# Kernel optimization log

Hardware: AMD Instinct MI355X
Metric: run time of the kernel (lower is better)

The kernel has to match this reference:

```python
import jax, jax.numpy as jnp
import numpy as np


def _glorot(key, shape):
    fan_in, fan_out = shape[0], shape[1]
    lim = float(np.sqrt(6.0 / (fan_in + fan_out)))
    return jax.random.uniform(key, shape, jnp.float32, -lim, lim)


def setup_inputs() -> dict:
    key = jax.random.key(0)
    ks = jax.random.split(key, 17)
    B, P, F = 32, 9045, 750  # batch, pairs-per-subject, feature dim
    x = jax.random.normal(ks[0], (B, P, F), jnp.float32)
    # SimilarityMeasureNetwork: 750 -> 32 -> 16 -> 8 -> 1
    sw1 = _glorot(ks[1], (750, 32)); sb1 = jnp.zeros((32,), jnp.float32)
    sw2 = _glorot(ks[2], (32, 16));  sb2 = jnp.zeros((16,), jnp.float32)
    sw3 = _glorot(ks[3], (16, 8));   sb3 = jnp.zeros((8,), jnp.float32)
    sw4 = _glorot(ks[4], (8, 1));    sb4 = jnp.zeros((1,), jnp.float32)
    # ClassificationNet: 9045 -> 1024 -> 256 -> 64 -> 3
    cw1 = _glorot(ks[5], (9045, 1024)); cb1 = jnp.zeros((1024,), jnp.float32)
    cw2 = _glorot(ks[6], (1024, 256));  cb2 = jnp.zeros((256,), jnp.float32)
    cw3 = _glorot(ks[7], (256, 64));    cb3 = jnp.zeros((64,), jnp.float32)
    cw4 = _glorot(ks[8], (64, 3));      cb4 = jnp.zeros((3,), jnp.float32)
    return dict(x=x, sw1=sw1, sb1=sb1, sw2=sw2, sb2=sb2, sw3=sw3, sb3=sb3,
                sw4=sw4, sb4=sb4, cw1=cw1, cb1=cb1, cw2=cw2, cb2=cb2,
                cw3=cw3, cb3=cb3, cw4=cw4, cb4=cb4)


def reference(x, sw1, sb1, sw2, sb2, sw3, sb3, sw4, sb4,
              cw1, cb1, cw2, cb2, cw3, cb3, cw4, cb4):
    # Similarity MLP, batched over all (subject, pair) rows at once.
    # Dropout layers are identity at inference.
    h = jax.nn.relu(jnp.einsum('bpf,fk->bpk', x, sw1) + sb1)   # [B,P,32]
    h = jax.nn.relu(h @ sw2 + sb2)                              # [B,P,16]
    h = jax.nn.relu(h @ sw3 + sb3)                              # [B,P,8]
    sim = jnp.tanh(h @ sw4 + sb4)[..., 0]                        # [B,P]
    # Classification MLP on the per-subject similarity vector.
    c = jax.nn.relu(sim @ cw1 + cb1)                             # [B,1024]
    c = jax.nn.relu(c @ cw2 + cb2)                               # [B,256]
    c = jax.nn.relu(c @ cw3 + cb3)                               # [B,64]
    logits = c @ cw4 + cb4                                       # [B,3]
    return jax.nn.log_softmax(logits, axis=1)
```

## Files before the change

kernel.cpp:

```cpp
#include <hip/hip_runtime.h>
#include <stdint.h>
#include <stddef.h>

#define BB 32
#define PP 9045
#define FF 750
#define MM (BB*PP)
#define NT16 (MM/16)

typedef float  f32x4  __attribute__((ext_vector_type(4)));
typedef short  s16x8  __attribute__((ext_vector_type(8)));
typedef unsigned int u32x4v __attribute__((ext_vector_type(4)));

typedef const __attribute__((address_space(1))) void* gp1;
typedef __attribute__((address_space(3))) void* sp3;
typedef __attribute__((address_space(3))) unsigned char* sp3c;

__device__ __forceinline__ unsigned rne_bf16(float f){
    unsigned u = __builtin_bit_cast(unsigned, f);
    return (u + 0x7fffu + ((u >> 16) & 1u)) >> 16;
}
__device__ __forceinline__ unsigned pack2(float lo, float hi){
    return rne_bf16(lo) | (rne_bf16(hi) << 16);
}
__device__ __forceinline__ unsigned cvtpk(float lo, float hi){
    unsigned r;
    asm volatile("v_cvt_pk_bf16_f32 %0, %1, %2" : "=v"(r) : "v"(lo), "v"(hi));
    return r;
}
__device__ __forceinline__ float tanh_fast(float v){
    return 1.f - 2.f / (1.f + __expf(2.f * v));
}

__global__ void k_w1f(const float* __restrict__ sw1, u32x4v* __restrict__ w1f){
    int t = blockIdx.x * blockDim.x + threadIdx.x;
    if (t >= 24*2*64) return;
    int lane = t & 63, nt = (t >> 6) & 1, s = t >> 7;
    int col = nt*16 + (lane & 15);
    int kb  = s*32 + ((lane >> 4) << 3);
    float v[8];
    #pragma unroll
    for (int e = 0; e < 8; ++e){ int k = kb + e; v[e] = (k < FF) ? sw1[k*32 + col] : 0.f; }
    u32x4v o;
    o.x = pack2(v[0],v[1]); o.y = pack2(v[2],v[3]);
    o.z = pack2(v[4],v[5]); o.w = pack2(v[6],v[7]);
    w1f[t] = o;
}

__global__ __launch_bounds__(256) void k_sim(
    const float* __restrict__ x, const u32x4v* __restrict__ w1f,
    const float* __restrict__ sb1,
    const float* __restrict__ sw2, const float* __restrict__ sb2,
    const float* __restrict__ sw3, const float* __restrict__ sb3,
    const float* __restrict__ sw4, const float* __restrict__ sb4,
    float* __restrict__ simT)
{
    __shared__ __attribute__((aligned(16))) unsigned char scratch[4*6144];
    const int wid  = threadIdx.x >> 6;
    const int lane = threadIdx.x & 63;
    const int tile = blockIdx.x*4 + wid;
    if (tile >= NT16) return;
    const int g = lane >> 4;
    const int c = lane & 15;
    const int r0 = tile << 4;
    const unsigned wbase = (unsigned)wid * 6144u;

    u32x4v t2, t3;
    {
        float v[8];
        #pragma unroll
        for (int e = 0; e < 8; ++e) v[e] = sw2[(8*g+e)*16 + c];
        t2.x = pack2(v[0],v[1]); t2.y = pack2(v[2],v[3]);
        t2.z = pack2(v[4],v[5]); t2.w = pack2(v[6],v[7]);
        #pragma unroll
        for (int e = 0; e < 8; ++e){
            int k = 8*g+e;
            v[e] = (k < 16 && c < 8) ? sw3[k*8 + c] : 0.f;
        }
        t3.x = pack2(v[0],v[1]); t3.y = pack2(v[2],v[3]);
        t3.z = pack2(v[4],v[5]); t3.w = pack2(v[6],v[7]);
    }
    const s16x8 w2f = __builtin_bit_cast(s16x8, t2);
    const s16x8 w3f = __builtin_bit_cast(s16x8, t3);
    const float w4c  = (c < 8) ? sw4[c] : 0.f;
    const float sb4v = sb4[0];
    const float b2c  = sb2[c];
    const float b3c  = (c < 8) ? sb3[c] : 0.f;

    f32x4 acc0, acc1;
    { float b0 = sb1[c], b1 = sb1[16+c];
      acc0 = (f32x4){b0,b0,b0,b0}; acc1 = (f32x4){b1,b1,b1,b1}; }

    const int rr = lane >> 3;
    const unsigned so = (unsigned)(((lane & 7) << 4) ^ ((rr & 3) << 4));
    const char* src0 = (const char*)x + (size_t)(r0 + rr) * 3000u + so;
    const char* src1 = src0 + 24000;

    unsigned char* ldsg = scratch;
    const uint32_t lbase = (uint32_t)(uintptr_t)(sp3c)scratch;
    const uint32_t sw = ((uint32_t)(c & 3)) << 4;
    const uint32_t rb0 = lbase + wbase + (uint32_t)c*128u + ((32u*(uint32_t)g) ^ sw);
    const uint32_t rb1 = lbase + wbase + (uint32_t)c*128u + (((32u*(uint32_t)g) + 16u) ^ sw);

    const unsigned long long wbw = (unsigned long long)(uintptr_t)w1f + (unsigned)lane*16u;

    u32x4v WA[3], WB[3];

#define GLLP(BUFOFS, STEP) do{ \
    __builtin_amdgcn_global_load_lds((gp1)(src0 + 128*(STEP)), (sp3)(ldsg + wbase + (BUFOFS)), 16, 0, 0); \
    __builtin_amdgcn_global_load_lds((gp1)(src1 + 128*(STEP)), (sp3)(ldsg + wbase + (BUFOFS) + 1024), 16, 0, 0); \
}while(0)

#define W1FLD(SLOT, STEP) do{ \
    unsigned long long wa_ = wbw + (unsigned)(2048*(STEP)); \
    asm volatile("global_load_dwordx4 %0, %1, off" : "=&v"(WA[SLOT]) : "v"(wa_)); \
    asm volatile("global_load_dwordx4 %0, %1, off offset:1024" : "=&v"(WB[SLOT]) : "v"(wa_)); \
}while(0)

#define PACK_MFMA(D0, D1, SLOT) do{ \
    u32x4v a_; \
    a_.x = cvtpk((D0)[0], (D0)[1]); a_.y = cvtpk((D0)[2], (D0)[3]); \
    a_.z = cvtpk((D1)[0], (D1)[1]); a_.w = cvtpk((D1)[2], (D1)[3]); \
    s16x8 av_ = __builtin_bit_cast(s16x8, a_); \
    acc0 = __builtin_amdgcn_mfma_f32_16x16x32_bf16(av_, __builtin_bit_cast(s16x8, WA[SLOT]), acc0, 0,0,0); \
    acc1 = __builtin_amdgcn_mfma_f32_16x16x32_bf16(av_, __builtin_bit_cast(s16x8, WB[SLOT]), acc1, 0,0,0); \
}while(0)

    GLLP(0,    0);
    W1FLD(0,   0);
    GLLP(2048, 1);
    W1FLD(1,   1);
    GLLP(4096, 2);

#pragma unroll
    for (int s = 0; s < 21; ++s){
        asm volatile("s_waitcnt vmcnt(6)");
        f32x4 d0, d1;
        const uint32_t off = (uint32_t)((s % 3) * 2048);
        asm volatile("ds_read_b128 %0, %1" : "=v"(d0) : "v"(rb0 + off));
        asm volatile("ds_read_b128 %0, %1" : "=v"(d1) : "v"(rb1 + off));
        W1FLD((s + 2) % 3, s + 2);
        asm volatile("s_waitcnt lgkmcnt(0)");
        __builtin_amdgcn_sched_barrier(0);
        if (s < 20) GLLP((s % 3) * 2048, s + 3);
        PACK_MFMA(d0, d1, s % 3);
    }
    {
        asm volatile("s_waitcnt vmcnt(4)");
        f32x4 d0, d1;
        asm volatile("ds_read_b128 %0, %1" : "=v"(d0) : "v"(rb0));
        asm volatile("ds_read_b128 %0, %1" : "=v"(d1) : "v"(rb1));
        W1FLD(2, 23);
        asm volatile("s_waitcnt lgkmcnt(0)");
        __builtin_amdgcn_sched_barrier(0);
        PACK_MFMA(d0, d1, 0);
    }
    {
        asm volatile("s_waitcnt vmcnt(2)");
        f32x4 d0, d1;
        asm volatile("ds_read_b128 %0, %1" : "=v"(d0) : "v"(rb0 + 2048u));
        asm volatile("ds_read_b128 %0, %1" : "=v"(d1) : "v"(rb1 + 2048u));
        asm volatile("s_waitcnt lgkmcnt(0)" ::: "memory");
        __builtin_amdgcn_sched_barrier(0);
        PACK_MFMA(d0, d1, 1);
    }
    {
        asm volatile("s_waitcnt vmcnt(0)" ::: "memory");
        __builtin_amdgcn_sched_barrier(0);
        int kb = 736 + g*8;
        float v[8];
        #pragma unroll
        for (int e = 0; e < 8; ++e){
            int k = kb + e;
            v[e] = (k < FF) ? x[(size_t)(r0 + c)*FF + k] : 0.f;
        }
        u32x4v a;
        a.x = pack2(v[0],v[1]); a.y = pack2(v[2],v[3]);
        a.z = pack2(v[4],v[5]); a.w = pack2(v[6],v[7]);
        s16x8 av = __builtin_bit_cast(s16x8, a);
        acc0 = __builtin_amdgcn_mfma_f32_16x16x32_bf16(av, __builtin_bit_cast(s16x8, WA[2]), acc0, 0,0,0);
        acc1 = __builtin_amdgcn_mfma_f32_16x16x32_bf16(av, __builtin_bit_cast(s16x8, WB[2]), acc1, 0,0,0);
    }

    unsigned short* h1 = (unsigned short*)(scratch + wbase);
    unsigned short* h2 = (unsigned short*)(scratch + wbase + 2048);
    for (int i = lane; i < 640; i += 64) h2[i] = 0;

    #pragma unroll
    for (int j = 0; j < 4; ++j){
        h1[(4*g+j)*40 + c]      = (unsigned short)rne_bf16(fmaxf(acc0[j], 0.f));
        h1[(4*g+j)*40 + 16 + c] = (unsigned short)rne_bf16(fmaxf(acc1[j], 0.f));
    }
    asm volatile("s_waitcnt lgkmcnt(0)" ::: "memory");
    s16x8 a2 = *reinterpret_cast<const s16x8*>(&h1[c*40 + 8*g]);
    f32x4 c2i = {b2c,b2c,b2c,b2c};
    f32x4 d2 = __builtin_amdgcn_mfma_f32_16x16x32_bf16(a2, w2f, c2i, 0,0,0);

    #pragma unroll
    for (int j = 0; j < 4; ++j)
        h2[(4*g+j)*40 + c] = (unsigned short)rne_bf16(fmaxf(d2[j], 0.f));
    asm volatile("s_waitcnt lgkmcnt(0)" ::: "memory");
    s16x8 a3 = *reinterpret_cast<const s16x8*>(&h2[c*40 + 8*g]);
    f32x4 c3i = {b3c,b3c,b3c,b3c};
    f32x4 d3 = __builtin_amdgcn_mfma_f32_16x16x32_bf16(a3, w3f, c3i, 0,0,0);

    #pragma unroll
    for (int j = 0; j < 4; ++j){
        float t = fmaxf(d3[j], 0.f) * w4c;
        t += __shfl_xor(t, 1);
        t += __shfl_xor(t, 2);
        t += __shfl_xor(t, 4);
        t += __shfl_xor(t, 8);
        if (c == 0){
            int grow = r0 + 4*g + j;
            int b = grow / PP;
            int p = grow - b*PP;
            simT[p*32 + b] = tanh_fast(t + sb4v);
        }
    }
#undef GLLP
#undef W1FLD
#undef PACK_MFMA
}

__global__ __launch_bounds__(256) void k_c1(
    const float* __restrict__ simT, const float* __restrict__ cw1,
    float* __restrict__ part)
{
    const int nb = blockIdx.x & 7;
    const int ks = blockIdx.x >> 3;
    const int t  = threadIdx.x;
    const int n  = nb*128 + (t & 127);
    const int kh = t >> 7;
    const int k0 = ks*283;
    const int k1 = (k0 + 283 < PP) ? k0 + 283 : PP;
    float acc[BB];
    #pragma unroll
    for (int b = 0; b < BB; ++b) acc[b] = 0.f;
    for (int k = k0 + kh; k < k1; k += 2){
        float w = cw1[(size_t)k*1024 + n];
        const float* sp = simT + k*32;
        #pragma unroll
        for (int b = 0; b < BB; ++b) acc[b] = fmaf(sp[b], w, acc[b]);
    }
    float* dst = part + (size_t)((ks << 1) | kh) * (BB * 1024) + n;
    #pragma unroll
    for (int b = 0; b < BB; ++b) dst[b*1024] = acc[b];
}

__global__ __launch_bounds__(256) void k_cls(
    const float* __restrict__ part, const float* __restrict__ cb1,
    const float* __restrict__ cw2,  const float* __restrict__ cb2,
    const float* __restrict__ cw3,  const float* __restrict__ cb3,
    const float* __restrict__ cw4,  const float* __restrict__ cb4,
    float* __restrict__ out)
{
    __shared__ __attribute__((aligned(16))) float c1s[1024];
    __shared__ float c2s[256];
    __shared__ float c3s[64];
    __shared__ float lgs[3];
    const int b = blockIdx.x, t = threadIdx.x;
    #pragma unroll
    for (int i = 0; i < 4; ++i){
        int n = i*256 + t;
        float a = 0.f;
        #pragma unroll 8
        for (int q = 0; q < 64; ++q) a += part[(size_t)q*(BB*1024) + b*1024 + n];
        c1s[n] = fmaxf(a + cb1[n], 0.f);
    }
    __syncthreads();
    {
        float a = cb2[t];
        for (int k = 0; k < 1024; k += 4){
            float4 cv = *reinterpret_cast<const float4*>(&c1s[k]);
            a = fmaf(cv.x, cw2[(k+0)*256 + t], a);
            a = fmaf(cv.y, cw2[(k+1)*256 + t], a);
            a = fmaf(cv.z, cw2[(k+2)*256 + t], a);
            a = fmaf(cv.w, cw2[(k+3)*256 + t], a);
        }
        c2s[t] = fmaxf(a, 0.f);
    }
    __syncthreads();
    if (t < 64){
        float a = cb3[t];
        for (int k = 0; k < 256; ++k) a = fmaf(c2s[k], cw3[k*64 + t], a);
        c3s[t] = fmaxf(a, 0.f);
    }
    __syncthreads();
    if (t < 3){
        float a = cb4[t];
        for (int k = 0; k < 64; ++k) a = fmaf(c3s[k], cw4[k*3 + t], a);
        lgs[t] = a;
    }
    __syncthreads();
    if (t < 3){
        float m = fmaxf(fmaxf(lgs[0], lgs[1]), lgs[2]);
        float s = __expf(lgs[0]-m) + __expf(lgs[1]-m) + __expf(lgs[2]-m);
        out[b*3 + t] = lgs[t] - m - __logf(s);
    }
}

extern "C" void kernel_launch(void* const* d_in, const int* in_sizes, int n_in,
                              void* d_out, int out_size, void* d_ws, size_t ws_size,
                              hipStream_t stream) {
    const float* x   = (const float*)d_in[0];
    const float* sw1 = (const float*)d_in[1];
    const float* sb1 = (const float*)d_in[2];
    const float* sw2 = (const float*)d_in[3];
    const float* sb2 = (const float*)d_in[4];
    const float* sw3 = (const float*)d_in[5];
    const float* sb3 = (const float*)d_in[6];
    const float* sw4 = (const float*)d_in[7];
    const float* sb4 = (const float*)d_in[8];
    const float* cw1 = (const float*)d_in[9];
    const float* cb1 = (const float*)d_in[10];
    const float* cw2 = (const float*)d_in[11];
    const float* cb2 = (const float*)d_in[12];
    const float* cw3 = (const float*)d_in[13];
    const float* cb3 = (const float*)d_in[14];
    const float* cw4 = (const float*)d_in[15];
    const float* cb4 = (const float*)d_in[16];
    (void)in_sizes; (void)n_in; (void)out_size; (void)ws_size;

    char* ws = (char*)d_ws;
    u32x4v* w1f  = (u32x4v*)ws;
    float*  simT = (float*)(ws + (64<<10));
    float*  part = (float*)(ws + (2<<20));

    k_w1f<<<12, 256, 0, stream>>>(sw1, w1f);
    k_sim<<<(NT16 + 3)/4, 256, 0, stream>>>(x, w1f, sb1, sw2, sb2, sw3, sb3,
                                            sw4, sb4, simT);
    k_c1 <<<256, 256, 0, stream>>>(simT, cw1, part);
    k_cls<<<BB, 256, 0, stream>>>(part, cb1, cw2, cb2, cw3, cb3, cw4, cb4,
                                  (float*)d_out);
}
```

Measured before the change: 358.4 us.

## Make similarity kernel persistent with whole-tile LDS staging and split-K across waves

Replaces the per-wave pipelined k_sim with a persistent kernel of 512 blocks. Each block stages a full 16-row x tile into LDS, and each wave keeps its share of W1 fragments resident in registers. The four waves split the K dimension, reduce partial accumulators through LDS, and wave 0 runs the small tail MLP. This is meant to avoid reloading W1 per tile, at the cost of losing the per-wave load/compute overlap and adding block-wide barriers and large LDS usage.

```diff
diff --git a/kernel.cpp b/kernel.cpp
--- a/kernel.cpp
+++ b/kernel.cpp
@@ -7,6 +7,7 @@
 #define FF 750
 #define MM (BB*PP)
 #define NT16 (MM/16)
+#define NBLK2 512
 
 typedef float  f32x4  __attribute__((ext_vector_type(4)));
 typedef short  s16x8  __attribute__((ext_vector_type(8)));
@@ -55,15 +56,20 @@
     const float* __restrict__ sw4, const float* __restrict__ sb4,
     float* __restrict__ simT)
 {
-    __shared__ __attribute__((aligned(16))) unsigned char scratch[4*6144];
-    const int wid  = threadIdx.x >> 6;
-    const int lane = threadIdx.x & 63;
-    const int tile = blockIdx.x*4 + wid;
-    if (tile >= NT16) return;
+    __shared__ __attribute__((aligned(16))) unsigned char scratch[58368];
+    const int tid  = threadIdx.x;
+    const int w    = tid >> 6;
+    const int lane = tid & 63;
     const int g = lane >> 4;
     const int c = lane & 15;
-    const int r0 = tile << 4;
-    const unsigned wbase = (unsigned)wid * 6144u;
+
+    u32x4v WA[6], WB[6];
+    #pragma unroll
+    for (int i = 0; i < 6; ++i){
+        int s = 6*w + i;
+        WA[i] = w1f[(2*s+0)*64 + lane];
+        WB[i] = w1f[(2*s+1)*64 + lane];
+    }
 
     u32x4v t2, t3;
     {
@@ -86,141 +92,119 @@
     const float sb4v = sb4[0];
     const float b2c  = sb2[c];
     const float b3c  = (c < 8) ? sb3[c] : 0.f;
-
-    f32x4 acc0, acc1;
-    { float b0 = sb1[c], b1 = sb1[16+c];
-      acc0 = (f32x4){b0,b0,b0,b0}; acc1 = (f32x4){b1,b1,b1,b1}; }
-
-    const int rr = lane >> 3;
-    const unsigned so = (unsigned)(((lane & 7) << 4) ^ ((rr & 3) << 4));
-    const char* src0 = (const char*)x + (size_t)(r0 + rr) * 3000u + so;
-    const char* src1 = src0 + 24000;
-
-    unsigned char* ldsg = scratch;
+    const float b1lo = sb1[c], b1hi = sb1[16+c];
+
+    {
+        unsigned short* h2z = (unsigned short*)(scratch + 50176);
+        for (int i = tid; i < 640; i += 256) h2z[i] = 0;
+    }
+
     const uint32_t lbase = (uint32_t)(uintptr_t)(sp3c)scratch;
-    const uint32_t sw = ((uint32_t)(c & 3)) << 4;
-    const uint32_t rb0 = lbase + wbase + (uint32_t)c*128u + ((32u*(uint32_t)g) ^ sw);
-    const uint32_t rb1 = lbase + wbase + (uint32_t)c*128u + (((32u*(uint32_t)g) + 16u) ^ sw);
-
-    const unsigned long long wbw = (unsigned long long)(uintptr_t)w1f + (unsigned)lane*16u;
-
-    u32x4v WA[3], WB[3];
-
-#define GLLP(BUFOFS, STEP) do{ \
-    __builtin_amdgcn_global_load_lds((gp1)(src0 + 128*(STEP)), (sp3)(ldsg + wbase + (BUFOFS)), 16, 0, 0); \
-    __builtin_amdgcn_global_load_lds((gp1)(src1 + 128*(STEP)), (sp3)(ldsg + wbase + (BUFOFS) + 1024), 16, 0, 0); \
+    const uint32_t rB = lbase + 3000u*(uint32_t)c + 32u*(uint32_t)g;
+
+#define STAGEW(BASE) do{ \
+    for (int j_ = w; j_ < 47; j_ += 4) \
+        __builtin_amdgcn_global_load_lds((gp1)((BASE) + 1024*j_ + 16*lane), \
+            (sp3)(scratch + 1024*j_), 16, 0, 0); \
 }while(0)
 
-#define W1FLD(SLOT, STEP) do{ \
-    unsigned long long wa_ = wbw + (unsigned)(2048*(STEP)); \
-    asm volatile("global_load_dwordx4 %0, %1, off" : "=&v"(WA[SLOT]) : "v"(wa_)); \
-    asm volatile("global_load_dwordx4 %0, %1, off offset:1024" : "=&v"(WB[SLOT]) : "v"(wa_)); \
-}while(0)
-
-#define PACK_MFMA(D0, D1, SLOT) do{ \
-    u32x4v a_; \
-    a_.x = cvtpk((D0)[0], (D0)[1]); a_.y = cvtpk((D0)[2], (D0)[3]); \
-    a_.z = cvtpk((D1)[0], (D1)[1]); a_.w = cvtpk((D1)[2], (D1)[3]); \
-    s16x8 av_ = __builtin_bit_cast(s16x8, a_); \
-    acc0 = __builtin_amdgcn_mfma_f32_16x16x32_bf16(av_, __builtin_bit_cast(s16x8, WA[SLOT]), acc0, 0,0,0); \
-    acc1 = __builtin_amdgcn_mfma_f32_16x16x32_bf16(av_, __builtin_bit_cast(s16x8, WB[SLOT]), acc1, 0,0,0); \
-}while(0)
-
-    GLLP(0,    0);
-    W1FLD(0,   0);
-    GLLP(2048, 1);
-    W1FLD(1,   1);
-    GLLP(4096, 2);
-
-#pragma unroll
-    for (int s = 0; s < 21; ++s){
-        asm volatile("s_waitcnt vmcnt(6)");
-        f32x4 d0, d1;
-        const uint32_t off = (uint32_t)((s % 3) * 2048);
-        asm volatile("ds_read_b128 %0, %1" : "=v"(d0) : "v"(rb0 + off));
-        asm volatile("ds_read_b128 %0, %1" : "=v"(d1) : "v"(rb1 + off));
-        W1FLD((s + 2) % 3, s + 2);
-        asm volatile("s_waitcnt lgkmcnt(0)");
-        __builtin_amdgcn_sched_barrier(0);
-        if (s < 20) GLLP((s % 3) * 2048, s + 3);
-        PACK_MFMA(d0, d1, s % 3);
-    }
-    {
-        asm volatile("s_waitcnt vmcnt(4)");
-        f32x4 d0, d1;
-        asm volatile("ds_read_b128 %0, %1" : "=v"(d0) : "v"(rb0));
-        asm volatile("ds_read_b128 %0, %1" : "=v"(d1) : "v"(rb1));
-        W1FLD(2, 23);
-        asm volatile("s_waitcnt lgkmcnt(0)");
-        __builtin_amdgcn_sched_barrier(0);
-        PACK_MFMA(d0, d1, 0);
-    }
-    {
-        asm volatile("s_waitcnt vmcnt(2)");
-        f32x4 d0, d1;
-        asm volatile("ds_read_b128 %0, %1" : "=v"(d0) : "v"(rb0 + 2048u));
-        asm volatile("ds_read_b128 %0, %1" : "=v"(d1) : "v"(rb1 + 2048u));
+    const char* cur = (const char*)x + 48000ull * (unsigned)blockIdx.x;
+
+    STAGEW(cur);
+    asm volatile("s_waitcnt vmcnt(0)" ::: "memory");
+    __syncthreads();
+
+    for (int t = blockIdx.x; t < NT16; t += NBLK2){
+        const char* nxt = cur + 48000ull * NBLK2;
+        const bool  pf  = (t + NBLK2 < NT16);
+        const int   r0  = t << 4;
+
+        f32x4 D0[6], D1[6];
+        #pragma unroll
+        for (int i = 0; i < 6; ++i){
+            uint32_t ad = rB + 128u*(uint32_t)(6*w + i);
+            asm volatile("ds_read_b128 %0, %1"           : "=&v"(D0[i]) : "v"(ad));
+            asm volatile("ds_read_b128 %0, %1 offset:16" : "=&v"(D1[i]) : "v"(ad));
+        }
         asm volatile("s_waitcnt lgkmcnt(0)" ::: "memory");
         __builtin_amdgcn_sched_barrier(0);
-        PACK_MFMA(d0, d1, 1);
-    }
-    {
+        if (w == 3){
+            if (g >= 2){ D0[5] = (f32x4){0.f,0.f,0.f,0.f}; D1[5] = (f32x4){0.f,0.f,0.f,0.f}; }
+            else if (g == 1){ D1[5][2] = 0.f; D1[5][3] = 0.f; }
+        }
+        f32x4 acc0, acc1;
+        if (w == 0){ acc0 = (f32x4){b1lo,b1lo,b1lo,b1lo}; acc1 = (f32x4){b1hi,b1hi,b1hi,b1hi}; }
+        else       { acc0 = (f32x4){0.f,0.f,0.f,0.f};     acc1 = (f32x4){0.f,0.f,0.f,0.f};     }
+        #pragma unroll
+        for (int i = 0; i < 6; ++i){
+            u32x4v a_;
+            a_.x = cvtpk(D0[i][0], D0[i][1]); a_.y = cvtpk(D0[i][2], D0[i][3]);
+            a_.z = cvtpk(D1[i][0], D1[i][1]); a_.w = cvtpk(D1[i][2], D1[i][3]);
+            s16x8 av = __builtin_bit_cast(s16x8, a_);
+            acc0 = __builtin_amdgcn_mfma_f32_16x16x32_bf16(av, __builtin_bit_cast(s16x8, WA[i]), acc0, 0,0,0);
+            acc1 = __builtin_amdgcn_mfma_f32_16x16x32_bf16(av, __builtin_bit_cast(s16x8, WB[i]), acc1, 0,0,0);
+        }
+
+        if (w){
+            float* cb = (float*)(scratch + 52224 + (unsigned)(w-1)*2048 + (unsigned)lane*32);
+            *(f32x4*)cb       = acc0;
+            *(f32x4*)(cb + 4) = acc1;
+        }
+        __syncthreads();
+
+        if (w == 0){
+            #pragma unroll
+            for (int q = 0; q < 3; ++q){
+                const float* cb = (const float*)(scratch + 52224 + (unsigned)q*2048 + (unsigned)lane*32);
+                f32x4 p0 = *(const f32x4*)cb;
+                f32x4 p1 = *(const f32x4*)(cb + 4);
+                #pragma unroll
+                for (int j = 0; j < 4; ++j){ acc0[j] += p0[j]; acc1[j] += p1[j]; }
+            }
+            unsigned short* h1 = (unsigned short*)(scratch + 48128);
+            unsigned short* h2 = (unsigned short*)(scratch + 50176);
+            #pragma unroll
+            for (int j = 0; j < 4; ++j){
+                h1[(4*g+j)*40 + c]      = (unsigned short)rne_bf16(fmaxf(acc0[j], 0.f));
+                h1[(4*g+j)*40 + 16 + c] = (unsigned short)rne_bf16(fmaxf(acc1[j], 0.f));
+            }
+            asm volatile("s_waitcnt lgkmcnt(0)" ::: "memory");
+            __builtin_amdgcn_sched_barrier(0);
+            s16x8 a2 = *reinterpret_cast<const s16x8*>(&h1[c*40 + 8*g]);
+            f32x4 c2i = {b2c,b2c,b2c,b2c};
+            f32x4 d2 = __builtin_amdgcn_mfma_f32_16x16x32_bf16(a2, w2f, c2i, 0,0,0);
+
+            #pragma unroll
+            for (int j = 0; j < 4; ++j)
+                h2[(4*g+j)*40 + c] = (unsigned short)rne_bf16(fmaxf(d2[j], 0.f));
+            asm volatile("s_waitcnt lgkmcnt(0)" ::: "memory");
+            __builtin_amdgcn_sched_barrier(0);
+            s16x8 a3 = *reinterpret_cast<const s16x8*>(&h2[c*40 + 8*g]);
+            f32x4 c3i = {b3c,b3c,b3c,b3c};
+            f32x4 d3 = __builtin_amdgcn_mfma_f32_16x16x32_bf16(a3, w3f, c3i, 0,0,0);
+
+            #pragma unroll
+            for (int j = 0; j < 4; ++j){
+                float tt = fmaxf(d3[j], 0.f) * w4c;
+                tt += __shfl_xor(tt, 1);
+                tt += __shfl_xor(tt, 2);
+                tt += __shfl_xor(tt, 4);
+                tt += __shfl_xor(tt, 8);
+                if (c == 0){
+                    int grow = r0 + 4*g + j;
+                    int b = grow / PP;
+                    int p = grow - b*PP;
+                    simT[p*32 + b] = tanh_fast(tt + sb4v);
+                }
+            }
+        }
+
+        if (pf) STAGEW(nxt);
         asm volatile("s_waitcnt vmcnt(0)" ::: "memory");
-        __builtin_amdgcn_sched_barrier(0);
-        int kb = 736 + g*8;
-        float v[8];
-        #pragma unroll
-        for (int e = 0; e < 8; ++e){
-            int k = kb + e;
-            v[e] = (k < FF) ? x[(size_t)(r0 + c)*FF + k] : 0.f;
-        }
-        u32x4v a;
-        a.x = pack2(v[0],v[1]); a.y = pack2(v[2],v[3]);
-        a.z = pack2(v[4],v[5]); a.w = pack2(v[6],v[7]);
-        s16x8 av = __builtin_bit_cast(s16x8, a);
-        acc0 = __builtin_amdgcn_mfma_f32_16x16x32_bf16(av, __builtin_bit_cast(s16x8, WA[2]), acc0, 0,0,0);
-        acc1 = __builtin_amdgcn_mfma_f32_16x16x32_bf16(av, __builtin_bit_cast(s16x8, WB[2]), acc1, 0,0,0);
-    }
-
-    unsigned short* h1 = (unsigned short*)(scratch + wbase);
-    unsigned short* h2 = (unsigned short*)(scratch + wbase + 2048);
-    for (int i = lane; i < 640; i += 64) h2[i] = 0;
-
-    #pragma unroll
-    for (int j = 0; j < 4; ++j){
-        h1[(4*g+j)*40 + c]      = (unsigned short)rne_bf16(fmaxf(acc0[j], 0.f));
-        h1[(4*g+j)*40 + 16 + c] = (unsigned short)rne_bf16(fmaxf(acc1[j], 0.f));
-    }
-    asm volatile("s_waitcnt lgkmcnt(0)" ::: "memory");
-    s16x8 a2 = *reinterpret_cast<const s16x8*>(&h1[c*40 + 8*g]);
-    f32x4 c2i = {b2c,b2c,b2c,b2c};
-    f32x4 d2 = __builtin_amdgcn_mfma_f32_16x16x32_bf16(a2, w2f, c2i, 0,0,0);
-
-    #pragma unroll
-    for (int j = 0; j < 4; ++j)
-        h2[(4*g+j)*40 + c] = (unsigned short)rne_bf16(fmaxf(d2[j], 0.f));
-    asm volatile("s_waitcnt lgkmcnt(0)" ::: "memory");
-    s16x8 a3 = *reinterpret_cast<const s16x8*>(&h2[c*40 + 8*g]);
-    f32x4 c3i = {b3c,b3c,b3c,b3c};
-    f32x4 d3 = __builtin_amdgcn_mfma_f32_16x16x32_bf16(a3, w3f, c3i, 0,0,0);
-
-    #pragma unroll
-    for (int j = 0; j < 4; ++j){
-        float t = fmaxf(d3[j], 0.f) * w4c;
-        t += __shfl_xor(t, 1);
-        t += __shfl_xor(t, 2);
-        t += __shfl_xor(t, 4);
-        t += __shfl_xor(t, 8);
-        if (c == 0){
-            int grow = r0 + 4*g + j;
-            int b = grow / PP;
-            int p = grow - b*PP;
-            simT[p*32 + b] = tanh_fast(t + sb4v);
-        }
-    }
-#undef GLLP
-#undef W1FLD
-#undef PACK_MFMA
+        __syncthreads();
+        cur = nxt;
+    }
+#undef STAGEW
 }
 
 __global__ __launch_bounds__(256) void k_c1(
@@ -328,8 +312,8 @@
     float*  part = (float*)(ws + (2<<20));
 
     k_w1f<<<12, 256, 0, stream>>>(sw1, w1f);
-    k_sim<<<(NT16 + 3)/4, 256, 0, stream>>>(x, w1f, sb1, sw2, sb2, sw3, sb3,
-                                            sw4, sb4, simT);
+    k_sim<<<NBLK2, 256, 0, stream>>>(x, w1f, sb1, sw2, sb2, sw3, sb3,
+                                     sw4, sb4, simT);
     k_c1 <<<256, 256, 0, stream>>>(simT, cw1, part);
     k_cls<<<BB, 256, 0, stream>>>(part, cb1, cw2, cb2, cw3, cb3, cw4, cb4,
                                   (float*)d_out);
```

Result: no change. 356.9 us (-0.4%).
